# Optimization experiments

Measured on AMD Instinct MI355X. Metric: run time of the kernel, lower is better.

The kernel has to match this reference:

```python
import jax, jax.numpy as jnp
import numpy as np

B = 16        # number of point clouds
N_PER = 2048  # points per cloud
K = 16        # knn neighbors
NUM_CLASSES = 40


def setup_inputs() -> dict:
    key = jax.random.key(0)
    ks = jax.random.split(key, 12)
    N = B * N_PER
    pos = jax.random.normal(ks[0], (N, 3), jnp.float32)
    normal = jax.random.normal(ks[1], (N, 3), jnp.float32)
    normal = normal / jnp.linalg.norm(normal, axis=1, keepdims=True)
    batch = jnp.arange(N, dtype=jnp.int32) // N_PER
    s = 0.1
    return {
        "pos": pos, "normal": normal, "batch": batch,
        # conv1 local_nn: Linear(4,32) -> ReLU -> Linear(32,32)
        "W1a": jax.random.normal(ks[2], (4, 32), jnp.float32) * s,
        "b1a": jnp.zeros((32,), jnp.float32),
        "W1b": jax.random.normal(ks[3], (32, 32), jnp.float32) * s,
        "b1b": jnp.zeros((32,), jnp.float32),
        # conv2 local_nn: Linear(36,32) -> ReLU -> Linear(32,32)
        "W2a": jax.random.normal(ks[4], (36, 32), jnp.float32) * s,
        "b2a": jnp.zeros((32,), jnp.float32),
        "W2b": jax.random.normal(ks[5], (32, 32), jnp.float32) * s,
        "b2b": jnp.zeros((32,), jnp.float32),
        # classifier: Linear(32, 40)
        "Wc": jax.random.normal(ks[6], (32, NUM_CLASSES), jnp.float32) * s,
        "bc": jnp.zeros((NUM_CLASSES,), jnp.float32),
    }


def _angle(v1, v2):
    cross = jnp.cross(v1, v2)
    return jnp.arctan2(jnp.linalg.norm(cross, axis=-1), jnp.sum(v1 * v2, axis=-1))


def _ppf(pos_i, pos_j, n_i, n_j):
    d = pos_j - pos_i
    return jnp.stack([
        jnp.linalg.norm(d, axis=-1),
        _angle(n_i, d),
        _angle(n_j, d),
        _angle(n_i, n_j),
    ], axis=-1)


def _mlp(x, Wa, ba, Wb, bb):
    return jax.nn.relu(x @ Wa + ba) @ Wb + bb


def reference(pos, normal, batch, W1a, b1a, W1b, b1b, W2a, b2a, W2b, b2b, Wc, bc):
    N = pos.shape[0]
    # --- knn_graph(k=16, loop=False) per cloud (equal-size clouds) ---
    p = pos.reshape(B, N_PER, 3)
    d2 = jnp.sum((p[:, :, None, :] - p[:, None, :, :]) ** 2, axis=-1)  # [B,n,n]
    d2 = jnp.where(jnp.eye(N_PER, dtype=bool), jnp.inf, d2)            # no self loop
    _, nbr = jax.lax.top_k(-d2, K)                                      # [B,n,K]
    nbr_g = (nbr + (jnp.arange(B) * N_PER)[:, None, None]).reshape(N, K)

    pos_j = pos[nbr_g]      # [N,K,3]
    n_j = normal[nbr_g]     # [N,K,3]
    ppf = _ppf(pos[:, None, :], pos_j, normal[:, None, :], n_j)  # [N,K,4]

    # conv1: message = PPF only (Linear(4,32)), max aggregation, relu
    h = jax.nn.relu(jnp.max(_mlp(ppf, W1a, b1a, W1b, b1b), axis=1))  # [N,32]
    # conv2: message = [h_j, ppf] (Linear(36,32)), max aggregation, relu
    msg2 = jnp.concatenate([h[nbr_g], ppf], axis=-1)                  # [N,K,36]
    h2 = jax.nn.relu(jnp.max(_mlp(msg2, W2a, b2a, W2b, b2b), axis=1))  # [N,32]

    # global max pool per cloud + classifier
    pooled = jnp.max(h2.reshape(B, N_PER, 32), axis=1)  # [B,32]
    return pooled @ Wc + bc
```

## Files before the change

kernel.cpp:

```cpp
#include <hip/hip_runtime.h>
#include <math.h>


#define NPER 2048
#define NCLOUD 16

#define OFF_NBR  (size_t)(0u)
#define OFF_PPF  (size_t)(2u << 20)
#define OFF_G    (size_t)(10u << 20)
#define OFF_POOL (size_t)(14u << 20)

__device__ __forceinline__ float med3(float a, float b, float c) {
    return __builtin_amdgcn_fmed3f(a, b, c);
}
__device__ __forceinline__ void cex(float& a, float& b) {
    const float lo = fminf(a, b), hi = fmaxf(a, b); a = lo; b = hi;
}
__device__ __forceinline__ void bmerge8(float (&v)[8]) {
#pragma unroll
    for (int i = 0; i < 4; ++i) cex(v[i], v[i + 4]);
#pragma unroll
    for (int b = 0; b < 8; b += 4)
#pragma unroll
        for (int i = 0; i < 2; ++i) cex(v[b + i], v[b + i + 2]);
#pragma unroll
    for (int b = 0; b < 8; b += 2) cex(v[b], v[b + 1]);
}
__device__ __forceinline__ void bmerge16(float (&v)[16]) {
#pragma unroll
    for (int i = 0; i < 8; ++i) cex(v[i], v[i + 8]);
#pragma unroll
    for (int b = 0; b < 16; b += 8)
#pragma unroll
        for (int i = 0; i < 4; ++i) cex(v[b + i], v[b + i + 4]);
#pragma unroll
    for (int b = 0; b < 16; b += 4)
#pragma unroll
        for (int i = 0; i < 2; ++i) cex(v[b + i], v[b + i + 2]);
#pragma unroll
    for (int b = 0; b < 16; b += 2) cex(v[b], v[b + 1]);
}

__device__ __forceinline__ float angf(float ax, float ay, float az,
                                      float bx, float by, float bz) {
    const float cx = ay * bz - az * by;
    const float cy = az * bx - ax * bz;
    const float cz = ax * by - ay * bx;
    const float cn = sqrtf(cx * cx + cy * cy + cz * cz);
    const float dt = ax * bx + ay * by + az * bz;
    return atan2f(cn, dt);
}

__global__ __launch_bounds__(256) void knn_conv1(const float* __restrict__ pos,
                                                 const float* __restrict__ nrm,
                                                 const float* __restrict__ W1a,
                                                 const float* __restrict__ b1a,
                                                 const float* __restrict__ W1b,
                                                 const float* __restrict__ b1b,
                                                 const float* __restrict__ W2a,
                                                 const float* __restrict__ b2a,
                                                 int* __restrict__ nbr,
                                                 float* __restrict__ ppf,
                                                 float* __restrict__ G) {
    const int tid = threadIdx.x;
    const int pl  = tid >> 4;
    const int sl  = tid & 15;
    const int gp  = blockIdx.x * 16 + pl;
    const int cloud = gp >> 11;
    const int lp  = gp & 2047;
    const int cbase = cloud * NPER;

    __shared__ float4 tile[2048];
    __shared__ int    hiL[16][40];
    __shared__ int    cnt[16];

    if (tid < 16) cnt[tid] = 0;

#pragma unroll
    for (int c = 0; c < 8; ++c) {
        const int idx = c * 256 + tid;
        const float x = pos[(cbase + idx) * 3 + 0];
        const float y = pos[(cbase + idx) * 3 + 1];
        const float z = pos[(cbase + idx) * 3 + 2];
        tile[idx] = make_float4(x, y, z, x * x + y * y + z * z);
    }
    __syncthreads();

    const float4 P  = tile[lp];
    const float pn2 = P.w;
    const float m2x = -2.f * P.x, m2y = -2.f * P.y, m2z = -2.f * P.z;

    float dl[4];
#pragma unroll
    for (int m = 0; m < 4; ++m) dl[m] = INFINITY;

#pragma unroll 4
    for (int jj = 0; jj < 128; ++jj) {
        const int cand = jj * 16 + sl;
        const float4 C = tile[cand];
        const float s = fmaf(m2x, C.x, fmaf(m2y, C.y, fmaf(m2z, C.z, C.w)));
        dl[3] = med3(dl[2], dl[3], s);
        dl[2] = med3(dl[1], dl[2], s);
        dl[1] = med3(dl[0], dl[1], s);
        dl[0] = fminf(dl[0], s);
    }
    if (sl == pl) {
        dl[0] = dl[1]; dl[1] = dl[2]; dl[2] = dl[3]; dl[3] = INFINITY;
    }

    float tau_s;
    {
        float v8[8];
#pragma unroll
        for (int i = 0; i < 4; ++i) v8[i] = dl[i];
#pragma unroll
        for (int i = 0; i < 4; ++i) v8[7 - i] = __shfl_xor(dl[i], 1);
        bmerge8(v8);
        float v[16];
#pragma unroll
        for (int i = 0; i < 8; ++i) v[i] = v8[i];
#pragma unroll
        for (int i = 0; i < 8; ++i) v[15 - i] = __shfl_xor(v8[i], 2);
        bmerge16(v);
        {
            float p[16];
#pragma unroll
            for (int i = 0; i < 16; ++i) p[i] = __shfl_xor(v[i], 4);
            float w[16];
#pragma unroll
            for (int i = 0; i < 16; ++i) w[i] = fminf(v[i], p[15 - i]);
            bmerge16(w);
#pragma unroll
            for (int i = 0; i < 16; ++i) v[i] = w[i];
        }
        {
            float p[16];
#pragma unroll
            for (int i = 0; i < 16; ++i) p[i] = __shfl_xor(v[i], 8);
            float t = -INFINITY;
#pragma unroll
            for (int i = 0; i < 16; ++i) t = fmaxf(t, fminf(v[i], p[15 - i]));
            tau_s = t;
        }
    }
    const float tsw = tau_s + 6e-5f * (1.f + pn2 + fabsf(tau_s + pn2));

#pragma unroll 4
    for (int jj = 0; jj < 128; ++jj) {
        const int cand = jj * 16 + sl;
        const float4 C = tile[cand];
        const float s = fmaf(m2x, C.x, fmaf(m2y, C.y, fmaf(m2z, C.z, C.w)));
        if (s <= tsw && cand != lp) {
            const int k = atomicAdd(&cnt[pl], 1);
            if (k < 40) hiL[pl][k] = cand;
        }
    }
    __syncthreads();

    if (tid < 16) {
        int n = cnt[tid];
        n = n > 40 ? 40 : n;
        if (n != 16) {
            const int myl = (blockIdx.x * 16 + tid) & 2047;
            const float4 Q = tile[myl];
            unsigned long long keys[16];
#pragma unroll
            for (int m = 0; m < 16; ++m) keys[m] = ~0ULL;
            for (int i = 0; i < n; ++i) {
                const int cand = hiL[tid][i];
                const float4 C = tile[cand];
                const float dx = __fsub_rn(Q.x, C.x);
                const float dy = __fsub_rn(Q.y, C.y);
                const float dz = __fsub_rn(Q.z, C.z);
                const float d2 = __fadd_rn(__fadd_rn(__fmul_rn(dx, dx),
                                                     __fmul_rn(dy, dy)),
                                           __fmul_rn(dz, dz));
                const unsigned long long key =
                    ((unsigned long long)__float_as_uint(d2) << 32) |
                    (unsigned int)cand;
                if (key < keys[15]) {
#pragma unroll
                    for (int m = 15; m >= 1; --m) {
                        const bool up   = key < keys[m - 1];
                        const bool here = key < keys[m];
                        keys[m] = up ? keys[m - 1] : (here ? key : keys[m]);
                    }
                    if (key < keys[0]) keys[0] = key;
                }
            }
#pragma unroll
            for (int m = 0; m < 16; ++m)
                hiL[tid][m] = (int)(unsigned int)(keys[m] & 0xFFFFFFFFu);
        }
    }
    __syncthreads();

    const float nix = nrm[gp * 3 + 0], niy = nrm[gp * 3 + 1], niz = nrm[gp * 3 + 2];
    float4 x;
    {
        const int jl = hiL[pl][sl];
        const int j  = cbase + jl;
        nbr[gp * 16 + sl] = j;
        const float4 C = tile[jl];
        const float njx = nrm[j * 3 + 0], njy = nrm[j * 3 + 1], njz = nrm[j * 3 + 2];
        const float dx = C.x - P.x, dy = C.y - P.y, dz = C.z - P.z;
        x.x = sqrtf(dx * dx + dy * dy + dz * dz);
        x.y = angf(nix, niy, niz, dx, dy, dz);
        x.z = angf(njx, njy, njz, dx, dy, dz);
        x.w = angf(nix, niy, niz, njx, njy, njz);
        ((float4*)ppf)[(size_t)gp * 16 + sl] = x;
    }

    float h1[32];
#pragma unroll
    for (int o = 0; o < 32; ++o) {
        h1[o] = fmaxf(fmaf(x.x, W1a[o],
                     fmaf(x.y, W1a[32 + o],
                     fmaf(x.z, W1a[64 + o],
                     fmaf(x.w, W1a[96 + o], b1a[o])))), 0.f);
    }

    float hr[32];
#pragma unroll 1
    for (int ob = 0; ob < 4; ++ob) {
        float acc[8];
#pragma unroll
        for (int u = 0; u < 8; ++u) acc[u] = b1b[ob * 8 + u];
#pragma unroll
        for (int hh = 0; hh < 32; ++hh) {
            const float hv = h1[hh];
#pragma unroll
            for (int u = 0; u < 8; ++u)
                acc[u] = fmaf(hv, W1b[hh * 32 + ob * 8 + u], acc[u]);
        }
#pragma unroll
        for (int u = 0; u < 8; ++u) {
            float v = acc[u];
            v = fmaxf(v, __shfl_xor(v, 1));
            v = fmaxf(v, __shfl_xor(v, 2));
            v = fmaxf(v, __shfl_xor(v, 4));
            v = fmaxf(v, __shfl_xor(v, 8));
            hr[ob * 8 + u] = fmaxf(v, 0.f);
        }
    }

    {
        const int c0 = sl * 2;
        float g0 = b2a[c0], g1 = b2a[c0 + 1];
#pragma unroll
        for (int k = 0; k < 32; ++k) {
            g0 = fmaf(hr[k], W2a[k * 32 + c0], g0);
            g1 = fmaf(hr[k], W2a[k * 32 + c0 + 1], g1);
        }
        ((float2*)(G + (size_t)gp * 32))[sl] = make_float2(g0, g1);
    }
}

#define SWZ(r) ((((r) & 7) ^ (((r) >> 4) & 7)) << 2)

__global__ __launch_bounds__(256) void conv2_pool(const float* __restrict__ ppf,
                                                  const int* __restrict__ nbr,
                                                  const float* __restrict__ G,
                                                  const float* __restrict__ W2a,
                                                  const float* __restrict__ W2b,
                                                  const float* __restrict__ b2b,
                                                  int* __restrict__ pooledi) {
    const int tid   = threadIdx.x;
    const int gid   = blockIdx.x * 256 + tid;
    const int cloud = blockIdx.x >> 7;

    __shared__ float M[256 * 32];
    __shared__ float sh[16][33];

    {
        const int j = nbr[gid];
        const float4 x = ((const float4*)ppf)[gid];
        const float4* gr = (const float4*)(G + (size_t)j * 32);
        const int wbase = tid * 32;
        const int swz = SWZ(tid);
#pragma unroll
        for (int q = 0; q < 8; ++q) {
            const float4 g = gr[q];
            float4 m4;
            m4.x = fmaxf(fmaf(x.x, W2a[32 * 32 + q * 4 + 0],
                        fmaf(x.y, W2a[33 * 32 + q * 4 + 0],
                        fmaf(x.z, W2a[34 * 32 + q * 4 + 0],
                        fmaf(x.w, W2a[35 * 32 + q * 4 + 0], g.x)))), 0.f);
            m4.y = fmaxf(fmaf(x.x, W2a[32 * 32 + q * 4 + 1],
                        fmaf(x.y, W2a[33 * 32 + q * 4 + 1],
                        fmaf(x.z, W2a[34 * 32 + q * 4 + 1],
                        fmaf(x.w, W2a[35 * 32 + q * 4 + 1], g.y)))), 0.f);
            m4.z = fmaxf(fmaf(x.x, W2a[32 * 32 + q * 4 + 2],
                        fmaf(x.y, W2a[33 * 32 + q * 4 + 2],
                        fmaf(x.z, W2a[34 * 32 + q * 4 + 2],
                        fmaf(x.w, W2a[35 * 32 + q * 4 + 2], g.z)))), 0.f);
            m4.w = fmaxf(fmaf(x.x, W2a[32 * 32 + q * 4 + 3],
                        fmaf(x.y, W2a[33 * 32 + q * 4 + 3],
                        fmaf(x.z, W2a[34 * 32 + q * 4 + 3],
                        fmaf(x.w, W2a[35 * 32 + q * 4 + 3], g.w)))), 0.f);
            *(float4*)&M[wbase + ((q * 4) ^ swz)] = m4;
        }
    }

    const int c0h = tid & 15;
    float2 w[32];
#pragma unroll
    for (int c = 0; c < 32; ++c) w[c] = ((const float2*)W2b)[c * 16 + c0h];
    const float2 bb = ((const float2*)b2b)[c0h];

    __syncthreads();

    const int node16 = tid >> 4;
    float mx0 = -INFINITY, mx1 = -INFINITY;
#pragma unroll 1
    for (int e = 0; e < 16; ++e) {
        const int r = (node16 << 4) + e;
        const int rbase = r * 32;
        const int swz = SWZ(r);
        float a0 = bb.x, a1 = bb.y;
#pragma unroll
        for (int cq = 0; cq < 8; ++cq) {
            const float4 m4 = *(const float4*)&M[rbase + ((cq * 4) ^ swz)];
            a0 = fmaf(m4.x, w[cq * 4 + 0].x, a0);
            a1 = fmaf(m4.x, w[cq * 4 + 0].y, a1);
            a0 = fmaf(m4.y, w[cq * 4 + 1].x, a0);
            a1 = fmaf(m4.y, w[cq * 4 + 1].y, a1);
            a0 = fmaf(m4.z, w[cq * 4 + 2].x, a0);
            a1 = fmaf(m4.z, w[cq * 4 + 2].y, a1);
            a0 = fmaf(m4.w, w[cq * 4 + 3].x, a0);
            a1 = fmaf(m4.w, w[cq * 4 + 3].y, a1);
        }
        mx0 = fmaxf(mx0, a0);
        mx1 = fmaxf(mx1, a1);
    }
    sh[node16][c0h * 2 + 0] = fmaxf(mx0, 0.f);
    sh[node16][c0h * 2 + 1] = fmaxf(mx1, 0.f);
    __syncthreads();

    if (tid < 32) {
        float m = sh[0][tid];
#pragma unroll
        for (int n = 1; n < 16; ++n) m = fmaxf(m, sh[n][tid]);
        atomicMax(&pooledi[cloud * 32 + tid], __float_as_int(m));
    }
}

__global__ __launch_bounds__(64) void fc_kernel(const int* __restrict__ pooledi,
                                                const float* __restrict__ Wc,
                                                const float* __restrict__ bc,
                                                float* __restrict__ out) {
    const int b = blockIdx.x;
    const int tid = threadIdx.x;
    if (tid < 40) {
        float acc = bc[tid];
#pragma unroll
        for (int o = 0; o < 32; ++o)
            acc = fmaf(__int_as_float(pooledi[b * 32 + o]), Wc[o * 40 + tid], acc);
        out[b * 40 + tid] = acc;
    }
}

extern "C" void kernel_launch(void* const* d_in, const int* in_sizes, int n_in,
                              void* d_out, int out_size, void* d_ws, size_t ws_size,
                              hipStream_t stream) {
    const float* pos = (const float*)d_in[0];
    const float* nrm = (const float*)d_in[1];
    const float* W1a = (const float*)d_in[3];
    const float* b1a = (const float*)d_in[4];
    const float* W1b = (const float*)d_in[5];
    const float* b1b = (const float*)d_in[6];
    const float* W2a = (const float*)d_in[7];
    const float* b2a = (const float*)d_in[8];
    const float* W2b = (const float*)d_in[9];
    const float* b2b = (const float*)d_in[10];
    const float* Wc  = (const float*)d_in[11];
    const float* bc  = (const float*)d_in[12];
    float* out = (float*)d_out;

    char* ws = (char*)d_ws;
    int*   nbr = (int*)(ws + OFF_NBR);
    float* ppf = (float*)(ws + OFF_PPF);
    float* G   = (float*)(ws + OFF_G);
    int*   pli = (int*)(ws + OFF_POOL);

    hipLaunchKernelGGL(knn_conv1,  dim3(2048), dim3(256), 0, stream,
                       pos, nrm, W1a, b1a, W1b, b1b, W2a, b2a, nbr, ppf, G);
    hipLaunchKernelGGL(conv2_pool, dim3(2048), dim3(256), 0, stream,
                       ppf, nbr, G, W2a, W2b, b2b, pli);
    hipLaunchKernelGGL(fc_kernel,  dim3(16),   dim3(64),  0, stream,
                       pli, Wc, bc, out);
}
```

Baseline: 184.5 us.

## Process two query points per thread group in knn_conv1 to amortize tile loads

Each block now handles 32 query points instead of 16, with every 16-lane group scanning candidates for two queries at once, so each shared-memory candidate read feeds two distance computations. The 8 KB-per-block cloud tile load from global memory is amortized over twice as many points, and the grid is halved. The cost is more registers for two top-4 lists and two thresholds, which may reduce occupancy. The second-pass refinement and MLP run serially over the two halves.

```diff
diff --git a/kernel.cpp b/kernel.cpp
--- a/kernel.cpp
+++ b/kernel.cpp
@@ -49,6 +49,41 @@
     const float cn = sqrtf(cx * cx + cy * cy + cz * cz);
     const float dt = ax * bx + ay * by + az * bz;
     return atan2f(cn, dt);
+}
+
+__device__ __forceinline__ float tau16(const float (&dl)[4]) {
+    float v8[8];
+#pragma unroll
+    for (int i = 0; i < 4; ++i) v8[i] = dl[i];
+#pragma unroll
+    for (int i = 0; i < 4; ++i) v8[7 - i] = __shfl_xor(dl[i], 1);
+    bmerge8(v8);
+    float v[16];
+#pragma unroll
+    for (int i = 0; i < 8; ++i) v[i] = v8[i];
+#pragma unroll
+    for (int i = 0; i < 8; ++i) v[15 - i] = __shfl_xor(v8[i], 2);
+    bmerge16(v);
+    {
+        float p[16];
+#pragma unroll
+        for (int i = 0; i < 16; ++i) p[i] = __shfl_xor(v[i], 4);
+        float w[16];
+#pragma unroll
+        for (int i = 0; i < 16; ++i) w[i] = fminf(v[i], p[15 - i]);
+        bmerge16(w);
+#pragma unroll
+        for (int i = 0; i < 16; ++i) v[i] = w[i];
+    }
+    float t = -INFINITY;
+    {
+        float p[16];
+#pragma unroll
+        for (int i = 0; i < 16; ++i) p[i] = __shfl_xor(v[i], 8);
+#pragma unroll
+        for (int i = 0; i < 16; ++i) t = fmaxf(t, fminf(v[i], p[15 - i]));
+    }
+    return t;
 }
 
 __global__ __launch_bounds__(256) void knn_conv1(const float* __restrict__ pos,
@@ -65,16 +100,18 @@
     const int tid = threadIdx.x;
     const int pl  = tid >> 4;
     const int sl  = tid & 15;
-    const int gp  = blockIdx.x * 16 + pl;
-    const int cloud = gp >> 11;
-    const int lp  = gp & 2047;
+    const int gp0 = blockIdx.x * 32 + pl;
+    const int gp1 = gp0 + 16;
+    const int cloud = gp0 >> 11;
+    const int lp0 = gp0 & 2047;
+    const int lp1 = lp0 + 16;
     const int cbase = cloud * NPER;
 
     __shared__ float4 tile[2048];
-    __shared__ int    hiL[16][40];
-    __shared__ int    cnt[16];
-
-    if (tid < 16) cnt[tid] = 0;
+    __shared__ int    hiL[32][40];
+    __shared__ int    cnt[32];
+
+    if (tid < 32) cnt[tid] = 0;
 
 #pragma unroll
     for (int c = 0; c < 8; ++c) {
@@ -86,82 +123,63 @@
     }
     __syncthreads();
 
-    const float4 P  = tile[lp];
-    const float pn2 = P.w;
-    const float m2x = -2.f * P.x, m2y = -2.f * P.y, m2z = -2.f * P.z;
-
-    float dl[4];
-#pragma unroll
-    for (int m = 0; m < 4; ++m) dl[m] = INFINITY;
+    const float4 P0 = tile[lp0];
+    const float4 P1 = tile[lp1];
+    const float pn20 = P0.w, pn21 = P1.w;
+    const float m2x0 = -2.f * P0.x, m2y0 = -2.f * P0.y, m2z0 = -2.f * P0.z;
+    const float m2x1 = -2.f * P1.x, m2y1 = -2.f * P1.y, m2z1 = -2.f * P1.z;
+
+    float dla[4], dlb[4];
+#pragma unroll
+    for (int m = 0; m < 4; ++m) { dla[m] = INFINITY; dlb[m] = INFINITY; }
 
 #pragma unroll 4
     for (int jj = 0; jj < 128; ++jj) {
         const int cand = jj * 16 + sl;
         const float4 C = tile[cand];
-        const float s = fmaf(m2x, C.x, fmaf(m2y, C.y, fmaf(m2z, C.z, C.w)));
-        dl[3] = med3(dl[2], dl[3], s);
-        dl[2] = med3(dl[1], dl[2], s);
-        dl[1] = med3(dl[0], dl[1], s);
-        dl[0] = fminf(dl[0], s);
+        const float s0 = fmaf(m2x0, C.x, fmaf(m2y0, C.y, fmaf(m2z0, C.z, C.w)));
+        const float s1 = fmaf(m2x1, C.x, fmaf(m2y1, C.y, fmaf(m2z1, C.z, C.w)));
+        dla[3] = med3(dla[2], dla[3], s0);
+        dla[2] = med3(dla[1], dla[2], s0);
+        dla[1] = med3(dla[0], dla[1], s0);
+        dla[0] = fminf(dla[0], s0);
+        dlb[3] = med3(dlb[2], dlb[3], s1);
+        dlb[2] = med3(dlb[1], dlb[2], s1);
+        dlb[1] = med3(dlb[0], dlb[1], s1);
+        dlb[0] = fminf(dlb[0], s1);
     }
     if (sl == pl) {
-        dl[0] = dl[1]; dl[1] = dl[2]; dl[2] = dl[3]; dl[3] = INFINITY;
-    }
-
-    float tau_s;
-    {
-        float v8[8];
-#pragma unroll
-        for (int i = 0; i < 4; ++i) v8[i] = dl[i];
-#pragma unroll
-        for (int i = 0; i < 4; ++i) v8[7 - i] = __shfl_xor(dl[i], 1);
-        bmerge8(v8);
-        float v[16];
-#pragma unroll
-        for (int i = 0; i < 8; ++i) v[i] = v8[i];
-#pragma unroll
-        for (int i = 0; i < 8; ++i) v[15 - i] = __shfl_xor(v8[i], 2);
-        bmerge16(v);
-        {
-            float p[16];
-#pragma unroll
-            for (int i = 0; i < 16; ++i) p[i] = __shfl_xor(v[i], 4);
-            float w[16];
-#pragma unroll
-            for (int i = 0; i < 16; ++i) w[i] = fminf(v[i], p[15 - i]);
-            bmerge16(w);
-#pragma unroll
-            for (int i = 0; i < 16; ++i) v[i] = w[i];
-        }
-        {
-            float p[16];
-#pragma unroll
-            for (int i = 0; i < 16; ++i) p[i] = __shfl_xor(v[i], 8);
-            float t = -INFINITY;
-#pragma unroll
-            for (int i = 0; i < 16; ++i) t = fmaxf(t, fminf(v[i], p[15 - i]));
-            tau_s = t;
-        }
-    }
-    const float tsw = tau_s + 6e-5f * (1.f + pn2 + fabsf(tau_s + pn2));
+        dla[0] = dla[1]; dla[1] = dla[2]; dla[2] = dla[3]; dla[3] = INFINITY;
+        dlb[0] = dlb[1]; dlb[1] = dlb[2]; dlb[2] = dlb[3]; dlb[3] = INFINITY;
+    }
+
+    const float tau0 = tau16(dla);
+    const float tau1 = tau16(dlb);
+    const float tsw0 = tau0 + 6e-5f * (1.f + pn20 + fabsf(tau0 + pn20));
+    const float tsw1 = tau1 + 6e-5f * (1.f + pn21 + fabsf(tau1 + pn21));
 
 #pragma unroll 4
     for (int jj = 0; jj < 128; ++jj) {
         const int cand = jj * 16 + sl;
         const float4 C = tile[cand];
-        const float s = fmaf(m2x, C.x, fmaf(m2y, C.y, fmaf(m2z, C.z, C.w)));
-        if (s <= tsw && cand != lp) {
+        const float s0 = fmaf(m2x0, C.x, fmaf(m2y0, C.y, fmaf(m2z0, C.z, C.w)));
+        const float s1 = fmaf(m2x1, C.x, fmaf(m2y1, C.y, fmaf(m2z1, C.z, C.w)));
+        if (s0 <= tsw0 && cand != lp0) {
             const int k = atomicAdd(&cnt[pl], 1);
             if (k < 40) hiL[pl][k] = cand;
         }
+        if (s1 <= tsw1 && cand != lp1) {
+            const int k = atomicAdd(&cnt[pl + 16], 1);
+            if (k < 40) hiL[pl + 16][k] = cand;
+        }
     }
     __syncthreads();
 
-    if (tid < 16) {
+    if (tid < 32) {
         int n = cnt[tid];
         n = n > 40 ? 40 : n;
         if (n != 16) {
-            const int myl = (blockIdx.x * 16 + tid) & 2047;
+            const int myl = (blockIdx.x * 32 + tid) & 2047;
             const float4 Q = tile[myl];
             unsigned long long keys[16];
 #pragma unroll
@@ -195,64 +213,74 @@
     }
     __syncthreads();
 
-    const float nix = nrm[gp * 3 + 0], niy = nrm[gp * 3 + 1], niz = nrm[gp * 3 + 2];
-    float4 x;
-    {
-        const int jl = hiL[pl][sl];
-        const int j  = cbase + jl;
-        nbr[gp * 16 + sl] = j;
-        const float4 C = tile[jl];
-        const float njx = nrm[j * 3 + 0], njy = nrm[j * 3 + 1], njz = nrm[j * 3 + 2];
-        const float dx = C.x - P.x, dy = C.y - P.y, dz = C.z - P.z;
-        x.x = sqrtf(dx * dx + dy * dy + dz * dz);
-        x.y = angf(nix, niy, niz, dx, dy, dz);
-        x.z = angf(njx, njy, njz, dx, dy, dz);
-        x.w = angf(nix, niy, niz, njx, njy, njz);
-        ((float4*)ppf)[(size_t)gp * 16 + sl] = x;
-    }
-
-    float h1[32];
-#pragma unroll
-    for (int o = 0; o < 32; ++o) {
-        h1[o] = fmaxf(fmaf(x.x, W1a[o],
-                     fmaf(x.y, W1a[32 + o],
-                     fmaf(x.z, W1a[64 + o],
-                     fmaf(x.w, W1a[96 + o], b1a[o])))), 0.f);
-    }
-
-    float hr[32];
 #pragma unroll 1
-    for (int ob = 0; ob < 4; ++ob) {
-        float acc[8];
-#pragma unroll
-        for (int u = 0; u < 8; ++u) acc[u] = b1b[ob * 8 + u];
-#pragma unroll
-        for (int hh = 0; hh < 32; ++hh) {
-            const float hv = h1[hh];
-#pragma unroll
-            for (int u = 0; u < 8; ++u)
-                acc[u] = fmaf(hv, W1b[hh * 32 + ob * 8 + u], acc[u]);
-        }
-#pragma unroll
-        for (int u = 0; u < 8; ++u) {
-            float v = acc[u];
-            v = fmaxf(v, __shfl_xor(v, 1));
-            v = fmaxf(v, __shfl_xor(v, 2));
-            v = fmaxf(v, __shfl_xor(v, 4));
-            v = fmaxf(v, __shfl_xor(v, 8));
-            hr[ob * 8 + u] = fmaxf(v, 0.f);
-        }
-    }
-
-    {
-        const int c0 = sl * 2;
-        float g0 = b2a[c0], g1 = b2a[c0 + 1];
-#pragma unroll
-        for (int k = 0; k < 32; ++k) {
-            g0 = fmaf(hr[k], W2a[k * 32 + c0], g0);
-            g1 = fmaf(hr[k], W2a[k * 32 + c0 + 1], g1);
-        }
-        ((float2*)(G + (size_t)gp * 32))[sl] = make_float2(g0, g1);
+    for (int half = 0; half < 2; ++half) {
+        const int pslot = pl + half * 16;
+        const int gp    = half ? gp1 : gp0;
+        const int lp    = half ? lp1 : lp0;
+        const float4 P  = half ? P1 : P0;
+
+        const float nix = nrm[gp * 3 + 0], niy = nrm[gp * 3 + 1],
+                    niz = nrm[gp * 3 + 2];
+        float4 x;
+        {
+            const int jl = hiL[pslot][sl];
+            const int j  = cbase + jl;
+            nbr[gp * 16 + sl] = j;
+            const float4 C = tile[jl];
+            const float njx = nrm[j * 3 + 0], njy = nrm[j * 3 + 1],
+                        njz = nrm[j * 3 + 2];
+            const float dx = C.x - P.x, dy = C.y - P.y, dz = C.z - P.z;
+            x.x = sqrtf(dx * dx + dy * dy + dz * dz);
+            x.y = angf(nix, niy, niz, dx, dy, dz);
+            x.z = angf(njx, njy, njz, dx, dy, dz);
+            x.w = angf(nix, niy, niz, njx, njy, njz);
+            ((float4*)ppf)[(size_t)gp * 16 + sl] = x;
+        }
+
+        float h1[32];
+#pragma unroll
+        for (int o = 0; o < 32; ++o) {
+            h1[o] = fmaxf(fmaf(x.x, W1a[o],
+                         fmaf(x.y, W1a[32 + o],
+                         fmaf(x.z, W1a[64 + o],
+                         fmaf(x.w, W1a[96 + o], b1a[o])))), 0.f);
+        }
+
+        float hr[32];
+#pragma unroll 1
+        for (int ob = 0; ob < 4; ++ob) {
+            float acc[8];
+#pragma unroll
+            for (int u = 0; u < 8; ++u) acc[u] = b1b[ob * 8 + u];
+#pragma unroll
+            for (int hh = 0; hh < 32; ++hh) {
+                const float hv = h1[hh];
+#pragma unroll
+                for (int u = 0; u < 8; ++u)
+                    acc[u] = fmaf(hv, W1b[hh * 32 + ob * 8 + u], acc[u]);
+            }
+#pragma unroll
+            for (int u = 0; u < 8; ++u) {
+                float v = acc[u];
+                v = fmaxf(v, __shfl_xor(v, 1));
+                v = fmaxf(v, __shfl_xor(v, 2));
+                v = fmaxf(v, __shfl_xor(v, 4));
+                v = fmaxf(v, __shfl_xor(v, 8));
+                hr[ob * 8 + u] = fmaxf(v, 0.f);
+            }
+        }
+
+        {
+            const int c0 = sl * 2;
+            float g0 = b2a[c0], g1 = b2a[c0 + 1];
+#pragma unroll
+            for (int k = 0; k < 32; ++k) {
+                g0 = fmaf(hr[k], W2a[k * 32 + c0], g0);
+                g1 = fmaf(hr[k], W2a[k * 32 + c0 + 1], g1);
+            }
+            ((float2*)(G + (size_t)gp * 32))[sl] = make_float2(g0, g1);
+        }
     }
 }
 
@@ -383,7 +411,7 @@
     float* G   = (float*)(ws + OFF_G);
     int*   pli = (int*)(ws + OFF_POOL);
 
-    hipLaunchKernelGGL(knn_conv1,  dim3(2048), dim3(256), 0, stream,
+    hipLaunchKernelGGL(knn_conv1,  dim3(1024), dim3(256), 0, stream,
                        pos, nrm, W1a, b1a, W1b, b1b, W2a, b2a, nbr, ppf, G);
     hipLaunchKernelGGL(conv2_pool, dim3(2048), dim3(256), 0, stream,
                        ppf, nbr, G, W2a, W2b, b2b, pli);
```

Measured after the change: 205.3 us. 1.11x slower.

## Stage cloud positions as packed float3 tile and use direct squared distances

Applied to the files above, without the earlier changes.

The shared tile now holds packed xyz (float3) instead of float4 with a precomputed norm, loaded with coalesced float4 vector copies. This shrinks shared memory from 32KB to 24KB, which may allow more blocks per CU. The candidate scan computes true squared distances instead of the norm-expanded form, which allows a tighter relative threshold and a smaller candidate buffer (24 instead of 40). The trade-offs are one extra operation per candidate and a risk of dropping true neighbors when the buffer overflows, for example on distance ties.

```diff
diff --git a/kernel.cpp b/kernel.cpp
--- a/kernel.cpp
+++ b/kernel.cpp
@@ -49,6 +49,41 @@
     const float cn = sqrtf(cx * cx + cy * cy + cz * cz);
     const float dt = ax * bx + ay * by + az * bz;
     return atan2f(cn, dt);
+}
+
+__device__ __forceinline__ float tau16(const float (&dl)[4]) {
+    float v8[8];
+#pragma unroll
+    for (int i = 0; i < 4; ++i) v8[i] = dl[i];
+#pragma unroll
+    for (int i = 0; i < 4; ++i) v8[7 - i] = __shfl_xor(dl[i], 1);
+    bmerge8(v8);
+    float v[16];
+#pragma unroll
+    for (int i = 0; i < 8; ++i) v[i] = v8[i];
+#pragma unroll
+    for (int i = 0; i < 8; ++i) v[15 - i] = __shfl_xor(v8[i], 2);
+    bmerge16(v);
+    {
+        float p[16];
+#pragma unroll
+        for (int i = 0; i < 16; ++i) p[i] = __shfl_xor(v[i], 4);
+        float w[16];
+#pragma unroll
+        for (int i = 0; i < 16; ++i) w[i] = fminf(v[i], p[15 - i]);
+        bmerge16(w);
+#pragma unroll
+        for (int i = 0; i < 16; ++i) v[i] = w[i];
+    }
+    float t = -INFINITY;
+    {
+        float p[16];
+#pragma unroll
+        for (int i = 0; i < 16; ++i) p[i] = __shfl_xor(v[i], 8);
+#pragma unroll
+        for (int i = 0; i < 16; ++i) t = fmaxf(t, fminf(v[i], p[15 - i]));
+    }
+    return t;
 }
 
 __global__ __launch_bounds__(256) void knn_conv1(const float* __restrict__ pos,
@@ -70,25 +105,21 @@
     const int lp  = gp & 2047;
     const int cbase = cloud * NPER;
 
-    __shared__ float4 tile[2048];
-    __shared__ int    hiL[16][40];
+    __shared__ float4 tile4[1536];
+    __shared__ int    hiL[16][24];
     __shared__ int    cnt[16];
+    const float3* xyz = (const float3*)tile4;
 
     if (tid < 16) cnt[tid] = 0;
 
-#pragma unroll
-    for (int c = 0; c < 8; ++c) {
-        const int idx = c * 256 + tid;
-        const float x = pos[(cbase + idx) * 3 + 0];
-        const float y = pos[(cbase + idx) * 3 + 1];
-        const float z = pos[(cbase + idx) * 3 + 2];
-        tile[idx] = make_float4(x, y, z, x * x + y * y + z * z);
-    }
-    __syncthreads();
-
-    const float4 P  = tile[lp];
-    const float pn2 = P.w;
-    const float m2x = -2.f * P.x, m2y = -2.f * P.y, m2z = -2.f * P.z;
+    {
+        const float4* src = (const float4*)(pos + (size_t)cbase * 3);
+#pragma unroll
+        for (int c = 0; c < 6; ++c) tile4[c * 256 + tid] = src[c * 256 + tid];
+    }
+    __syncthreads();
+
+    const float3 P = xyz[lp];
 
     float dl[4];
 #pragma unroll
@@ -97,78 +128,46 @@
 #pragma unroll 4
     for (int jj = 0; jj < 128; ++jj) {
         const int cand = jj * 16 + sl;
-        const float4 C = tile[cand];
-        const float s = fmaf(m2x, C.x, fmaf(m2y, C.y, fmaf(m2z, C.z, C.w)));
-        dl[3] = med3(dl[2], dl[3], s);
-        dl[2] = med3(dl[1], dl[2], s);
-        dl[1] = med3(dl[0], dl[1], s);
-        dl[0] = fminf(dl[0], s);
+        const float3 C = xyz[cand];
+        const float dx = C.x - P.x, dy = C.y - P.y, dz = C.z - P.z;
+        const float d2 = fmaf(dz, dz, fmaf(dy, dy, dx * dx));
+        dl[3] = med3(dl[2], dl[3], d2);
+        dl[2] = med3(dl[1], dl[2], d2);
+        dl[1] = med3(dl[0], dl[1], d2);
+        dl[0] = fminf(dl[0], d2);
     }
     if (sl == pl) {
         dl[0] = dl[1]; dl[1] = dl[2]; dl[2] = dl[3]; dl[3] = INFINITY;
     }
 
-    float tau_s;
-    {
-        float v8[8];
-#pragma unroll
-        for (int i = 0; i < 4; ++i) v8[i] = dl[i];
-#pragma unroll
-        for (int i = 0; i < 4; ++i) v8[7 - i] = __shfl_xor(dl[i], 1);
-        bmerge8(v8);
-        float v[16];
-#pragma unroll
-        for (int i = 0; i < 8; ++i) v[i] = v8[i];
-#pragma unroll
-        for (int i = 0; i < 8; ++i) v[15 - i] = __shfl_xor(v8[i], 2);
-        bmerge16(v);
-        {
-            float p[16];
-#pragma unroll
-            for (int i = 0; i < 16; ++i) p[i] = __shfl_xor(v[i], 4);
-            float w[16];
-#pragma unroll
-            for (int i = 0; i < 16; ++i) w[i] = fminf(v[i], p[15 - i]);
-            bmerge16(w);
-#pragma unroll
-            for (int i = 0; i < 16; ++i) v[i] = w[i];
-        }
-        {
-            float p[16];
-#pragma unroll
-            for (int i = 0; i < 16; ++i) p[i] = __shfl_xor(v[i], 8);
-            float t = -INFINITY;
-#pragma unroll
-            for (int i = 0; i < 16; ++i) t = fmaxf(t, fminf(v[i], p[15 - i]));
-            tau_s = t;
-        }
-    }
-    const float tsw = tau_s + 6e-5f * (1.f + pn2 + fabsf(tau_s + pn2));
+    const float tau_s = tau16(dl);
+    const float tsw = fmaf(tau_s, 4e-5f, tau_s) + 1e-20f;
 
 #pragma unroll 4
     for (int jj = 0; jj < 128; ++jj) {
         const int cand = jj * 16 + sl;
-        const float4 C = tile[cand];
-        const float s = fmaf(m2x, C.x, fmaf(m2y, C.y, fmaf(m2z, C.z, C.w)));
-        if (s <= tsw && cand != lp) {
+        const float3 C = xyz[cand];
+        const float dx = C.x - P.x, dy = C.y - P.y, dz = C.z - P.z;
+        const float d2 = fmaf(dz, dz, fmaf(dy, dy, dx * dx));
+        if (d2 <= tsw && cand != lp) {
             const int k = atomicAdd(&cnt[pl], 1);
-            if (k < 40) hiL[pl][k] = cand;
+            if (k < 24) hiL[pl][k] = cand;
         }
     }
     __syncthreads();
 
     if (tid < 16) {
         int n = cnt[tid];
-        n = n > 40 ? 40 : n;
+        n = n > 24 ? 24 : n;
         if (n != 16) {
             const int myl = (blockIdx.x * 16 + tid) & 2047;
-            const float4 Q = tile[myl];
+            const float3 Q = xyz[myl];
             unsigned long long keys[16];
 #pragma unroll
             for (int m = 0; m < 16; ++m) keys[m] = ~0ULL;
             for (int i = 0; i < n; ++i) {
                 const int cand = hiL[tid][i];
-                const float4 C = tile[cand];
+                const float3 C = xyz[cand];
                 const float dx = __fsub_rn(Q.x, C.x);
                 const float dy = __fsub_rn(Q.y, C.y);
                 const float dz = __fsub_rn(Q.z, C.z);
@@ -201,7 +200,7 @@
         const int jl = hiL[pl][sl];
         const int j  = cbase + jl;
         nbr[gp * 16 + sl] = j;
-        const float4 C = tile[jl];
+        const float3 C = xyz[jl];
         const float njx = nrm[j * 3 + 0], njy = nrm[j * 3 + 1], njz = nrm[j * 3 + 2];
         const float dx = C.x - P.x, dy = C.y - P.y, dz = C.z - P.z;
         x.x = sqrtf(dx * dx + dy * dy + dz * dz);
```

After: 187.2 us. No clear change (+1.5%).
